# Performance work log

Measured on AMD Instinct MI355X. Metric: run time of the kernel, lower is better.

## Reference

```python
import jax, jax.numpy as jnp
import numpy as np
from jax import lax

ALPHA = 0.9
LN_EPS = 1e-3  # keras LayerNormalization default epsilon


def ema(x, a):
    # x: [..., T, D]; ema[0]=x[0], ema[i]=a*x[i]+(1-a)*ema[i-1]
    xt = jnp.moveaxis(x, -2, 0)  # [T, ..., D]
    def step(carry, xi):
        y = a * xi + (1.0 - a) * carry
        return y, y
    y0 = xt[0]
    _, ys = lax.scan(step, y0, xt[1:])
    out = jnp.concatenate([y0[None], ys], axis=0)
    return jnp.moveaxis(out, 0, -2)


def setup_inputs() -> dict:
    key = jax.random.key(0)
    ks = jax.random.split(key, 5)
    B, T, D = 32, 256, 512
    s = lambda fan: 1.0 / np.sqrt(fan)
    return {
        "x": jax.random.normal(ks[0], (B, T, D), jnp.float32),
        "W1": jax.random.normal(ks[1], (D, T), jnp.float32) * s(D),
        "b1": jnp.zeros((T,), jnp.float32),
        "W2": jax.random.normal(ks[2], (T, T), jnp.float32) * s(T),
        "b2": jnp.zeros((T,), jnp.float32),
        "W3": jax.random.normal(ks[3], (T, T), jnp.float32) * s(T),
        "b3": jnp.zeros((T,), jnp.float32),
        "gamma": jnp.ones((T * T,), jnp.float32),
        "beta": jnp.zeros((T * T,), jnp.float32),
        "Wa": jax.random.normal(ks[4], (T * T, T), jnp.float32) * s(T * T),
        "ba": jnp.zeros((T,), jnp.float32),
    }


def reference(x, W1, b1, W2, b2, W3, b3, gamma, beta, Wa, ba):
    B, T, D = x.shape
    # Two chained EMA passes with elementwise add
    e1 = ema(x, ALPHA)
    e = e1 + ema(e1, ALPHA * 1.5)
    # idx_attn: Dense(tanh) -> Dense(relu) -> Dense(linear) -> Flatten -> LayerNorm
    h = jnp.tanh(jnp.einsum("btd,dc->btc", e, W1) + b1)       # [B,T,T]
    h = jax.nn.relu(jnp.einsum("btc,cd->btd", h, W2) + b2)
    h = jnp.einsum("btc,cd->btd", h, W3) + b3
    f = h.reshape(B, T * T)
    mu = jnp.mean(f, axis=-1, keepdims=True)
    var = jnp.mean(jnp.square(f - mu), axis=-1, keepdims=True)
    f = (f - mu) * lax.rsqrt(var + LN_EPS) * gamma + beta
    # w_attn: EinsumDense '...b,bc->...c' with sigmoid
    g = jax.nn.sigmoid(f @ Wa + ba)                            # [B,T]
    return g[..., None] * x
```

## Files before the change

kernel.cpp:

```cpp
#include <hip/hip_runtime.h>
#include <hip/hip_bf16.h>

#define B_ 32
#define T_ 256
#define D_ 512
#define L_ (T_ * T_)

typedef __attribute__((ext_vector_type(8))) short bf16x8;
typedef __attribute__((ext_vector_type(4))) float f32x4;

static __device__ __forceinline__ unsigned short f2bf(float f) {
  __hip_bfloat16 h = __float2bfloat16(f);
  return *reinterpret_cast<unsigned short*>(&h);
}

__global__ __launch_bounds__(256) void convert_wt(const float* __restrict__ W,
                                                  __hip_bfloat16* __restrict__ Wt,
                                                  int K, int N) {
  __shared__ float tile[32][33];
  const int k0 = blockIdx.y * 32, n0 = blockIdx.x * 32;
  const int c = threadIdx.x & 31, r = threadIdx.x >> 5;
#pragma unroll
  for (int i = 0; i < 32; i += 8)
    tile[r + i][c] = W[(size_t)(k0 + r + i) * N + n0 + c];
  __syncthreads();
#pragma unroll
  for (int i = 0; i < 32; i += 8)
    Wt[(size_t)(n0 + r + i) * K + k0 + c] = __float2bfloat16(tile[c][r + i]);
}

#define EMA_CH 32
__global__ __launch_bounds__(128) void ema2_kernel(const float* __restrict__ x,
                                                   __hip_bfloat16* __restrict__ e) {
  const int flat = blockIdx.x * 128 + threadIdx.x;
  const int d4 = flat & 127;
  const int ci = (flat >> 7) & 7;
  const int b = flat >> 10;
  const double a1d = 0.9, a2d = 0.9 * 1.5;
  const float a1 = (float)a1d, o1 = (float)(1.0 - a1d);
  const float a2 = (float)a2d, o2 = (float)(1.0 - a2d);

  const size_t base = (size_t)b * (T_ * D_) + (size_t)d4 * 4;
  const float* xp = x + base;
  __hip_bfloat16* ep = e + base;

  f32x4 c1, c2;
  const int t0 = ci * EMA_CH;
  int tstart;
  if (ci == 0) {
    const f32x4 xv = *(const f32x4*)xp;
    c1 = xv;
    c2 = xv;
    const f32x4 v = c1 + c2;
    short4 p;
    p.x = (short)f2bf(v.x); p.y = (short)f2bf(v.y);
    p.z = (short)f2bf(v.z); p.w = (short)f2bf(v.w);
    *(short4*)ep = p;
    tstart = 1;
  } else {
    c1 = (f32x4){0.f, 0.f, 0.f, 0.f};
    c2 = (f32x4){0.f, 0.f, 0.f, 0.f};
#pragma unroll 8
    for (int t = t0 - EMA_CH; t < t0; ++t) {
      const f32x4 xv = *(const f32x4*)(xp + (size_t)t * D_);
      c1 = a1 * xv + o1 * c1;
      c2 = a2 * c1 + o2 * c2;
    }
    tstart = t0;
  }
#pragma unroll 8
  for (int t = tstart; t < t0 + EMA_CH; ++t) {
    const f32x4 xv = *(const f32x4*)(xp + (size_t)t * D_);
    c1 = a1 * xv + o1 * c1;
    c2 = a2 * c1 + o2 * c2;
    const f32x4 v = c1 + c2;
    short4 p;
    p.x = (short)f2bf(v.x); p.y = (short)f2bf(v.y);
    p.z = (short)f2bf(v.z); p.w = (short)f2bf(v.w);
    *(short4*)(ep + (size_t)t * D_) = p;
  }
}

template <int K, int ACT, bool OUTBF16>
__global__ __launch_bounds__(256) void mfma_gemm(const __hip_bfloat16* __restrict__ A,
                                                 const __hip_bfloat16* __restrict__ Bt,
                                                 const float* __restrict__ bias,
                                                 void* __restrict__ Cout, int N) {
  __shared__ __align__(16) short As[128 * 32];
  __shared__ __align__(16) short Bs[128 * 32];
  const int tid = threadIdx.x;
  const int lane = tid & 63, w = tid >> 6;
  const int wr = w >> 1, wc = w & 1;
  const int rowBase = blockIdx.y * 128, colBase = blockIdx.x * 128;
  const int r = tid >> 2, kb = tid & 3;

  const short* Ag = (const short*)A;
  const short* Bg = (const short*)Bt;

  f32x4 acc[4][4] = {};

  for (int k0 = 0; k0 < K; k0 += 32) {
    __builtin_amdgcn_global_load_lds(
        (const __attribute__((address_space(1))) void*)(Ag + (size_t)(rowBase + r) * K + k0 + kb * 8),
        (__attribute__((address_space(3))) void*)(As + w * 512), 16, 0, 0);
    __builtin_amdgcn_global_load_lds(
        (const __attribute__((address_space(1))) void*)(Ag + (size_t)(rowBase + 64 + r) * K + k0 + kb * 8),
        (__attribute__((address_space(3))) void*)(As + 2048 + w * 512), 16, 0, 0);
    __builtin_amdgcn_global_load_lds(
        (const __attribute__((address_space(1))) void*)(Bg + (size_t)(colBase + r) * K + k0 + kb * 8),
        (__attribute__((address_space(3))) void*)(Bs + w * 512), 16, 0, 0);
    __builtin_amdgcn_global_load_lds(
        (const __attribute__((address_space(1))) void*)(Bg + (size_t)(colBase + 64 + r) * K + k0 + kb * 8),
        (__attribute__((address_space(3))) void*)(Bs + 2048 + w * 512), 16, 0, 0);
    __syncthreads();

    bf16x8 af[4], bfr[4];
#pragma unroll
    for (int m = 0; m < 4; ++m)
      af[m] = *(const bf16x8*)&As[(wr * 64 + m * 16 + (lane & 15)) * 32 + (lane >> 4) * 8];
#pragma unroll
    for (int n = 0; n < 4; ++n)
      bfr[n] = *(const bf16x8*)&Bs[(wc * 64 + n * 16 + (lane & 15)) * 32 + (lane >> 4) * 8];
#pragma unroll
    for (int m = 0; m < 4; ++m)
#pragma unroll
      for (int n = 0; n < 4; ++n)
        acc[m][n] = __builtin_amdgcn_mfma_f32_16x16x32_bf16(af[m], bfr[n], acc[m][n], 0, 0, 0);
    __syncthreads();
  }

  const int orow0 = rowBase + wr * 64 + ((lane >> 4) << 2);
  const int ocol0 = colBase + wc * 64 + (lane & 15);
#pragma unroll
  for (int m = 0; m < 4; ++m)
#pragma unroll
    for (int n = 0; n < 4; ++n) {
      const int gc = ocol0 + n * 16;
      const float bv = bias[gc];
#pragma unroll
      for (int j = 0; j < 4; ++j) {
        const size_t gr = orow0 + m * 16 + j;
        float v = acc[m][n][j] + bv;
        if (ACT == 0) v = tanhf(v);
        if (ACT == 1) v = fmaxf(v, 0.f);
        if (OUTBF16)
          ((__hip_bfloat16*)Cout)[gr * N + gc] = __float2bfloat16(v);
        else
          ((float*)Cout)[gr * N + gc] = v;
      }
    }
}

__global__ __launch_bounds__(1024) void ln_stats_kernel(const float* __restrict__ f,
                                                        float* __restrict__ stats) {
  const int b = blockIdx.x;
  const f32x4* fp = (const f32x4*)(f + (size_t)b * L_);
  float s = 0.f, s2 = 0.f;
  for (int i = threadIdx.x; i < L_ / 4; i += 1024) {
    f32x4 v = fp[i];
    s += v.x + v.y + v.z + v.w;
    s2 += v.x * v.x + v.y * v.y + v.z * v.z + v.w * v.w;
  }
#pragma unroll
  for (int off = 32; off; off >>= 1) {
    s += __shfl_down(s, off, 64);
    s2 += __shfl_down(s2, off, 64);
  }
  __shared__ float ls[16], ls2[16];
  const int wid = threadIdx.x >> 6, lane = threadIdx.x & 63;
  if (lane == 0) { ls[wid] = s; ls2[wid] = s2; }
  __syncthreads();
  if (threadIdx.x == 0) {
    float S = 0.f, S2 = 0.f;
#pragma unroll
    for (int i = 0; i < 16; ++i) { S += ls[i]; S2 += ls2[i]; }
    const float mu = S / L_;
    const float var = S2 / L_ - mu * mu;
    stats[b * 2 + 0] = mu;
    stats[b * 2 + 1] = rsqrtf(var + 1e-3f);
  }
}

#define WKC 256
__global__ __launch_bounds__(256) void wa_gemm2(const float* __restrict__ f,
                                                const float* __restrict__ Wa,
                                                const float* __restrict__ gamma,
                                                const float* __restrict__ beta,
                                                const float* __restrict__ stats,
                                                float* __restrict__ partial) {
  const int kbidx = blockIdx.x;
  const int k0 = kbidx * WKC;
  const int tid = threadIdx.x, lane = tid & 63, w = tid >> 6;
  __shared__ float fs[WKC][36];

  for (int l = tid; l < B_ * WKC; l += 256) {
    const int b = l >> 8, kk = l & (WKC - 1);
    const int gk = k0 + kk;
    fs[kk][b] = (f[(size_t)b * L_ + gk] - stats[b * 2]) * stats[b * 2 + 1] * gamma[gk] + beta[gk];
  }
  __syncthreads();

  f32x4 acc[B_];
#pragma unroll
  for (int b = 0; b < B_; ++b) acc[b] = {0.f, 0.f, 0.f, 0.f};

  const int kbeg = w * 64;
  for (int kk = kbeg; kk < kbeg + 64; ++kk) {
    const f32x4 wv = *(const f32x4*)&Wa[(size_t)(k0 + kk) * T_ + lane * 4];
    const float* fr = fs[kk];
#pragma unroll
    for (int b = 0; b < B_; ++b) acc[b] += wv * fr[b];
  }

  float* red = &fs[0][0];
#pragma unroll
  for (int p = 0; p < 4; ++p) {
    __syncthreads();
#pragma unroll
    for (int b8 = 0; b8 < 8; ++b8)
      *(f32x4*)&red[(w * 8 + b8) * 256 + lane * 4] = acc[p * 8 + b8];
    __syncthreads();
#pragma unroll
    for (int i = 0; i < 8; ++i) {
      const int o = i * 256 + tid;
      const int b8 = o >> 8, n = o & 255;
      const float s = red[(0 * 8 + b8) * 256 + n] + red[(1 * 8 + b8) * 256 + n] +
                      red[(2 * 8 + b8) * 256 + n] + red[(3 * 8 + b8) * 256 + n];
      partial[(size_t)kbidx * (B_ * T_) + (p * 8 + b8) * T_ + n] = s;
    }
  }
}

__global__ __launch_bounds__(256) void wa_reduce(const float* __restrict__ partial,
                                                 const float* __restrict__ ba,
                                                 float* __restrict__ g) {
  const int o0 = blockIdx.x * 32;
  const int tid = threadIdx.x, lane = tid & 63, w = tid >> 6;
  const int oo = tid & 31;
  const int kg = tid >> 5;
  float s = 0.f;
#pragma unroll 8
  for (int i = 0; i < 32; ++i)
    s += partial[(size_t)(kg * 32 + i) * (B_ * T_) + o0 + oo];
  s += __shfl_down(s, 32, 64);
  __shared__ float red[4][32];
  if ((lane >> 5) == 0) red[w][oo] = s;
  __syncthreads();
  if (tid < 32) {
    float tot = red[0][tid] + red[1][tid] + red[2][tid] + red[3][tid];
    const int o = o0 + tid;
    tot += ba[o & (T_ - 1)];
    g[o] = 1.f / (1.f + __expf(-tot));
  }
}

__global__ __launch_bounds__(128) void finalize_kernel(const float* __restrict__ x,
                                                       const float* __restrict__ g,
                                                       float* __restrict__ out) {
  const int bt = blockIdx.x;
  const float sg = g[bt];
  const f32x4* xp = (const f32x4*)(x + (size_t)bt * D_);
  f32x4* op = (f32x4*)(out + (size_t)bt * D_);
  op[threadIdx.x] = xp[threadIdx.x] * sg;
}

extern "C" void kernel_launch(void* const* d_in, const int* in_sizes, int n_in,
                              void* d_out, int out_size, void* d_ws, size_t ws_size,
                              hipStream_t stream) {
  const float* x     = (const float*)d_in[0];
  const float* W1    = (const float*)d_in[1];
  const float* b1    = (const float*)d_in[2];
  const float* W2    = (const float*)d_in[3];
  const float* b2    = (const float*)d_in[4];
  const float* W3    = (const float*)d_in[5];
  const float* b3    = (const float*)d_in[6];
  const float* gamma = (const float*)d_in[7];
  const float* beta  = (const float*)d_in[8];
  const float* Wa    = (const float*)d_in[9];
  const float* ba    = (const float*)d_in[10];
  float* out = (float*)d_out;

  char* ws = (char*)d_ws;
  __hip_bfloat16* h1  = (__hip_bfloat16*)(ws + 0);
  __hip_bfloat16* h2  = (__hip_bfloat16*)(ws + 4194304);
  float* f            = (float*)(ws + 8388608);
  __hip_bfloat16* Wt1 = (__hip_bfloat16*)(ws + 16777216);
  __hip_bfloat16* Wt2 = (__hip_bfloat16*)(ws + 17039360);
  __hip_bfloat16* Wt3 = (__hip_bfloat16*)(ws + 17170432);
  float* stats        = (float*)(ws + 17301504);
  float* g            = (float*)(ws + 17301760);
  float* partial      = (float*)(ws + 0);
  __hip_bfloat16* e16 = (__hip_bfloat16*)d_out;

  convert_wt<<<dim3(T_ / 32, D_ / 32), 256, 0, stream>>>(W1, Wt1, D_, T_);
  convert_wt<<<dim3(T_ / 32, T_ / 32), 256, 0, stream>>>(W2, Wt2, T_, T_);
  convert_wt<<<dim3(T_ / 32, T_ / 32), 256, 0, stream>>>(W3, Wt3, T_, T_);
  ema2_kernel<<<(B_ * (T_ / EMA_CH) * (D_ / 4)) / 128, 128, 0, stream>>>(x, e16);
  mfma_gemm<D_, 0, true><<<dim3(T_ / 128, (B_ * T_) / 128), 256, 0, stream>>>(e16, Wt1, b1, h1, T_);
  mfma_gemm<T_, 1, true><<<dim3(T_ / 128, (B_ * T_) / 128), 256, 0, stream>>>(h1, Wt2, b2, h2, T_);
  mfma_gemm<T_, 2, false><<<dim3(T_ / 128, (B_ * T_) / 128), 256, 0, stream>>>(h2, Wt3, b3, f, T_);
  ln_stats_kernel<<<B_, 1024, 0, stream>>>(f, stats);
  wa_gemm2<<<L_ / WKC, 256, 0, stream>>>(f, Wa, gamma, beta, stats, partial);
  wa_reduce<<<(B_ * T_) / 32, 256, 0, stream>>>(partial, ba, g);
  finalize_kernel<<<B_ * T_, 128, 0, stream>>>(x, g, out);
}
```

Baseline: 233.9 us.

## Restructure Wa GEMM into 512-thread blocks with batch-split accumulators

Rewrites the LayerNorm-then-Wa GEMM kernel to use 512 threads per block. Each wave now handles 8 batch rows over half of the K chunk, instead of all 32 batch rows over a quarter. This drops the per-thread accumulators from 32 to 8 float4 vectors, which cuts register pressure and should raise occupancy. The reduction shrinks to a single two-way shared-memory add, and the f values are read from LDS with vector loads. In exchange, each Wa row is now loaded by four waves instead of one, which increases global and L2 traffic on Wa.

After: 226.8 us. -3.0%, faster.

```diff
diff --git a/kernel.cpp b/kernel.cpp
--- a/kernel.cpp
+++ b/kernel.cpp
@@ -182,7 +182,7 @@
 }
 
 #define WKC 256
-__global__ __launch_bounds__(256) void wa_gemm2(const float* __restrict__ f,
+__global__ __launch_bounds__(512) void wa_gemm3(const float* __restrict__ f,
                                                 const float* __restrict__ Wa,
                                                 const float* __restrict__ gamma,
                                                 const float* __restrict__ beta,
@@ -191,42 +191,49 @@
   const int kbidx = blockIdx.x;
   const int k0 = kbidx * WKC;
   const int tid = threadIdx.x, lane = tid & 63, w = tid >> 6;
+  const int g = w & 3, h = w >> 2;
   __shared__ float fs[WKC][36];
 
-  for (int l = tid; l < B_ * WKC; l += 256) {
+  for (int l = tid; l < B_ * WKC; l += 512) {
     const int b = l >> 8, kk = l & (WKC - 1);
     const int gk = k0 + kk;
     fs[kk][b] = (f[(size_t)b * L_ + gk] - stats[b * 2]) * stats[b * 2 + 1] * gamma[gk] + beta[gk];
   }
   __syncthreads();
 
-  f32x4 acc[B_];
-#pragma unroll
-  for (int b = 0; b < B_; ++b) acc[b] = {0.f, 0.f, 0.f, 0.f};
-
-  const int kbeg = w * 64;
-  for (int kk = kbeg; kk < kbeg + 64; ++kk) {
-    const f32x4 wv = *(const f32x4*)&Wa[(size_t)(k0 + kk) * T_ + lane * 4];
-    const float* fr = fs[kk];
-#pragma unroll
-    for (int b = 0; b < B_; ++b) acc[b] += wv * fr[b];
-  }
-
+  f32x4 acc[8] = {};
+  const int b0 = g * 8;
+  const size_t kbase = k0 + h * 128;
+  for (int kk = 0; kk < 128; kk += 4) {
+    f32x4 wv[4];
+#pragma unroll
+    for (int u = 0; u < 4; ++u)
+      wv[u] = *(const f32x4*)&Wa[(kbase + kk + u) * T_ + lane * 4];
+#pragma unroll
+    for (int u = 0; u < 4; ++u) {
+      const float* frow = &fs[h * 128 + kk + u][b0];
+      const f32x4 fA = *(const f32x4*)frow;
+      const f32x4 fB = *(const f32x4*)(frow + 4);
+      acc[0] += wv[u] * fA.x; acc[1] += wv[u] * fA.y;
+      acc[2] += wv[u] * fA.z; acc[3] += wv[u] * fA.w;
+      acc[4] += wv[u] * fB.x; acc[5] += wv[u] * fB.y;
+      acc[6] += wv[u] * fB.z; acc[7] += wv[u] * fB.w;
+    }
+  }
+
+  __syncthreads();
   float* red = &fs[0][0];
-#pragma unroll
-  for (int p = 0; p < 4; ++p) {
-    __syncthreads();
-#pragma unroll
-    for (int b8 = 0; b8 < 8; ++b8)
-      *(f32x4*)&red[(w * 8 + b8) * 256 + lane * 4] = acc[p * 8 + b8];
-    __syncthreads();
-#pragma unroll
-    for (int i = 0; i < 8; ++i) {
-      const int o = i * 256 + tid;
-      const int b8 = o >> 8, n = o & 255;
-      const float s = red[(0 * 8 + b8) * 256 + n] + red[(1 * 8 + b8) * 256 + n] +
-                      red[(2 * 8 + b8) * 256 + n] + red[(3 * 8 + b8) * 256 + n];
-      partial[(size_t)kbidx * (B_ * T_) + (p * 8 + b8) * T_ + n] = s;
+  if (h == 1) {
+#pragma unroll
+    for (int bb = 0; bb < 8; ++bb)
+      *(f32x4*)&red[(size_t)(b0 + bb) * 256 + lane * 4] = acc[bb];
+  }
+  __syncthreads();
+  if (h == 0) {
+#pragma unroll
+    for (int bb = 0; bb < 8; ++bb) {
+      const f32x4 o = acc[bb] + *(const f32x4*)&red[(size_t)(b0 + bb) * 256 + lane * 4];
+      *(f32x4*)&partial[(size_t)kbidx * (B_ * T_) + (size_t)(b0 + bb) * T_ + lane * 4] = o;
     }
   }
 }
@@ -300,7 +307,7 @@
   mfma_gemm<T_, 1, true><<<dim3(T_ / 128, (B_ * T_) / 128), 256, 0, stream>>>(h1, Wt2, b2, h2, T_);
   mfma_gemm<T_, 2, false><<<dim3(T_ / 128, (B_ * T_) / 128), 256, 0, stream>>>(h2, Wt3, b3, f, T_);
   ln_stats_kernel<<<B_, 1024, 0, stream>>>(f, stats);
-  wa_gemm2<<<L_ / WKC, 256, 0, stream>>>(f, Wa, gamma, beta, stats, partial);
+  wa_gemm3<<<L_ / WKC, 512, 0, stream>>>(f, Wa, gamma, beta, stats, partial);
   wa_reduce<<<(B_ * T_) / 32, 256, 0, stream>>>(partial, ba, g);
   finalize_kernel<<<B_ * T_, 128, 0, stream>>>(x, g, out);
 }
```
